# Optimization experiments

Measured on AMD Instinct MI355X. Metric: run time of the kernel, lower is better.

The kernel has to match this reference:

```python
import jax, jax.numpy as jnp
import numpy as np

B, N, DIM = 1, 512, 1024
HEADS, DH = 16, 64          # dim_head = 64, _dim = heads*dh = 1024
P = 32                      # projection_dim
P2 = P // 2
NEG_INF = -1e30


def setup_inputs() -> dict:
    key = jax.random.key(0)
    ks = jax.random.split(key, 14)
    s = 0.02
    _dim = HEADS * DH
    return {
        "x":    jax.random.normal(ks[0], (B, N, DIM), dtype=jnp.float32),
        "Wqkv": jax.random.normal(ks[1], (3 * _dim, DIM), dtype=jnp.float32) * s,
        "Wout": jax.random.normal(ks[2], (DIM, _dim), dtype=jnp.float32) * s,
        "Wq":   jax.random.normal(ks[3], (P, DH), dtype=jnp.float32) * s,
        "bq":   jax.random.normal(ks[4], (P,), dtype=jnp.float32) * s,
        "Wk":   jax.random.normal(ks[5], (P, DH), dtype=jnp.float32) * s,
        "bk":   jax.random.normal(ks[6], (P,), dtype=jnp.float32) * s,
        "W1":   jax.random.normal(ks[7], (P, 2 * P), dtype=jnp.float32) * s,
        "b1":   jax.random.normal(ks[8], (P,), dtype=jnp.float32) * s,
        "W2":   jax.random.normal(ks[9], (P2, P), dtype=jnp.float32) * s,
        "b2":   jax.random.normal(ks[10], (P2,), dtype=jnp.float32) * s,
        "W3":   jax.random.normal(ks[11], (1, P2), dtype=jnp.float32) * s,
        "b3":   jax.random.normal(ks[12], (1,), dtype=jnp.float32) * s,
    }


def reference(x, Wqkv, Wout, Wq, bq, Wk, bk, W1, b1, W2, b2, W3, b3):
    b, n, _ = x.shape
    # qkv projection, then einops 'b n (d k h) -> k b h n d' split (d outermost!)
    qkv = jnp.einsum('bnc,oc->bno', x, Wqkv).reshape(b, n, DH, 3, HEADS)
    q = jnp.transpose(qkv[:, :, :, 0, :], (0, 3, 1, 2))  # [b,h,n,dh]
    k = jnp.transpose(qkv[:, :, :, 1, :], (0, 3, 1, 2))
    v = jnp.transpose(qkv[:, :, :, 2, :], (0, 3, 1, 2))

    qp = jnp.einsum('bhnd,pd->bhnp', q, Wq) + bq  # [b,h,n,P]
    kp = jnp.einsum('bhnd,pd->bhnp', k, Wk) + bk

    # linear1 on concat(q_i, k_j): split W1 -> broadcast-add (same math,
    # avoids materializing the [b,h,n,n,2P] concat tensor)
    W1q, W1k = W1[:, :P], W1[:, P:]
    a = jnp.einsum('bhnp,qp->bhnq', qp, W1q)      # [b,h,n,P]
    c = jnp.einsum('bhnp,qp->bhnq', kp, W1k)      # [b,h,n,P]
    h1 = jax.nn.relu(a[:, :, :, None, :] + c[:, :, None, :, :] + b1)  # [b,h,n,n,P]
    h2 = jax.nn.relu(jnp.einsum('bhijp,qp->bhijq', h1, W2) + b2)      # [b,h,n,n,P/2]
    score = jnp.einsum('bhijq,oq->bhijo', h2, W3)[..., 0] + b3[0]     # [b,h,n,n]

    # causal mask (triu(1) filled with -inf)
    i = jnp.arange(n)
    causal = i[None, :] > i[:, None]
    score = jnp.where(causal, NEG_INF, score)

    attn = jax.nn.softmax(score, axis=-1)
    out = jnp.einsum('bhij,bhjd->bhid', attn, v)                      # [b,h,n,dh]
    out = jnp.transpose(out, (0, 2, 1, 3)).reshape(b, n, HEADS * DH)  # b n (h d)
    return jnp.einsum('bne,oe->bno', out, Wout)
```

## Files before the change

### kernel.cpp

```cpp
#include <hip/hip_runtime.h>
#include <hip/hip_bf16.h>
#include <hip/hip_fp16.h>
#include <math.h>

#define N_SEQ 512
#define DIM   1024
#define HEADS 16
#define DH    64
#define P     32
#define P2    16
#define PSTR  520

typedef short    bf16x8 __attribute__((ext_vector_type(8)));
typedef _Float16 f16x8  __attribute__((ext_vector_type(8)));
typedef float    f32x4  __attribute__((ext_vector_type(4)));

__device__ inline unsigned short f2bf(float f) {
  union { float f; unsigned u; } v; v.f = f;
  unsigned r = (v.u + 0x7fffu + ((v.u >> 16) & 1u)) >> 16;
  return (unsigned short)r;
}

union H8 { f16x8 v; __half2 h2[4]; unsigned u32[4]; };

__global__ __launch_bounds__(256) void prep(
    const float* __restrict__ Wqkv, const float* __restrict__ Wq,
    const float* __restrict__ bq, const float* __restrict__ Wk,
    const float* __restrict__ bk, const float* __restrict__ W1,
    const float* __restrict__ b1,
    const float* __restrict__ x, const float* __restrict__ Wout,
    short* __restrict__ Wcomb, short* __restrict__ xb,
    short* __restrict__ Woutb, float* __restrict__ ba32,
    float* __restrict__ bc32) {
  const int b = blockIdx.x, tid = threadIdx.x;
  if (b < 256) {
    __shared__ float W1s[32][33];
    __shared__ float Wqs[32][65];
    __shared__ float wsm[32][65];
    __shared__ __align__(16) float qsT[128][65];
    const int part = b >> 7, rem = b & 127;
    const int h = rem >> 3, c0 = (rem & 7) * 128;
    const int grow = part * 16 + h;
    for (int idx = tid; idx < 1024; idx += 256)
      W1s[idx >> 5][idx & 31] = W1[(idx >> 5) * 64 + part * 32 + (idx & 31)];
    const float* Wsel = part ? Wk : Wq;
    for (int idx = tid; idx < 2048; idx += 256)
      Wqs[idx >> 6][idx & 63] = Wsel[idx];
    for (int idx = tid; idx < 2048; idx += 256) {
      const int d = idx >> 5, c4 = idx & 31;
      const float4 v =
          *(const float4*)(Wqkv + (size_t)(d * 48 + grow) * DIM + c0 + c4 * 4);
      qsT[c4 * 4 + 0][d] = v.x;
      qsT[c4 * 4 + 1][d] = v.y;
      qsT[c4 * 4 + 2][d] = v.z;
      qsT[c4 * 4 + 3][d] = v.w;
    }
    __syncthreads();
    for (int idx = tid; idx < 2048; idx += 256) {
      const int q = idx >> 6, d = idx & 63;
      float s = 0.f;
#pragma unroll
      for (int p = 0; p < 32; ++p) s += W1s[q][p] * Wqs[p][d];
      wsm[q][d] = s;
    }
    __syncthreads();
    {
      const int c = tid & 127;
      float qr[64];
#pragma unroll
      for (int d4 = 0; d4 < 16; ++d4)
        *(float4*)&qr[d4 * 4] = *(const float4*)&qsT[c][d4 * 4];
#pragma unroll
      for (int step = 0; step < 16; ++step) {
        const int idx = step * 256 + tid;
        const int q = idx >> 7;
        float s = 0.f;
#pragma unroll
        for (int d = 0; d < 64; ++d) s += wsm[q][d] * qr[d];
        Wcomb[(size_t)(part * 512 + h * 32 + q) * DIM + c0 + c] = (short)f2bf(s);
      }
    }
    if (rem == 0 && tid < 32) {
      const float* bsel = part ? bk : bq;
      float s = 0.f;
#pragma unroll
      for (int p = 0; p < 32; ++p) s += W1s[tid][p] * bsel[p];
      if (part) s += b1[tid];
      (part ? bc32 : ba32)[tid] = s;
    }
  } else if (b < 384) {
#pragma unroll
    for (int rr = 0; rr < 8; ++rr) {
      const int ov = (b - 256) * 8 + rr;
      const int h = ov >> 6, d = ov & 63;
      const float4 v = *(const float4*)(Wqkv + (size_t)(d * 48 + 32 + h) * DIM + tid * 4);
      ushort4 o;
      o.x = f2bf(v.x); o.y = f2bf(v.y); o.z = f2bf(v.z); o.w = f2bf(v.w);
      *(ushort4*)(Wcomb + (size_t)(1024 + ov) * DIM + tid * 4) = o;
    }
  } else if (b < 512) {
    const int idx = (b - 384) * 256 + tid;
#pragma unroll
    for (int u = 0; u < 4; ++u) {
      const int t = u * 32768 + idx;
      const float4 v = ((const float4*)x)[t];
      ushort4 o;
      o.x = f2bf(v.x); o.y = f2bf(v.y); o.z = f2bf(v.z); o.w = f2bf(v.w);
      ((ushort4*)xb)[t] = o;
    }
  } else {
    const int idx = (b - 512) * 256 + tid;
#pragma unroll
    for (int u = 0; u < 4; ++u) {
      const int t = u * 65536 + idx;
      const float4 v = ((const float4*)Wout)[t];
      ushort4 o;
      o.x = f2bf(v.x); o.y = f2bf(v.y); o.z = f2bf(v.z); o.w = f2bf(v.w);
      ((ushort4*)Woutb)[t] = o;
    }
  }
}

__global__ __launch_bounds__(512) void gemm_acv(
    const short* __restrict__ xb, const short* __restrict__ Wcomb,
    const float* __restrict__ ba32, const float* __restrict__ bc32,
    __half* __restrict__ a_buf, __half* __restrict__ cb_buf,
    __half* __restrict__ vT) {
  const int bb = blockIdx.x;
  const int tm = bb >> 5;
  const int tn = bb & 31;
  const int w = threadIdx.x >> 6;
  const int wm = w >> 1, wn = w & 1;
  const int lane = threadIdx.x & 63;
  const int m = lane & 15, quad = lane >> 4;

  const int row0 = tm * 64 + wm * 16;
  const int col0 = tn * 64 + wn * 32;

  const short* pa  = xb + (size_t)(row0 + m) * DIM + quad * 8;
  const short* pb0 = Wcomb + (size_t)(col0 + m) * DIM + quad * 8;
  const short* pb1 = pb0 + (size_t)16 * DIM;

  bf16x8 abuf[4], b0buf[4], b1buf[4];
#pragma unroll
  for (int j = 0; j < 4; ++j) {
    abuf[j]  = *(const bf16x8*)(pa  + j * 32);
    b0buf[j] = *(const bf16x8*)(pb0 + j * 32);
    b1buf[j] = *(const bf16x8*)(pb1 + j * 32);
  }

  f32x4 acc0 = {0.f, 0.f, 0.f, 0.f}, acc1 = {0.f, 0.f, 0.f, 0.f};

#pragma unroll
  for (int ko = 0; ko < 8; ++ko) {
#pragma unroll
    for (int j = 0; j < 4; ++j) {
      const int k = ko * 4 + j;
      const bf16x8 av  = abuf[j];
      const bf16x8 b0v = b0buf[j];
      const bf16x8 b1v = b1buf[j];
      if (k + 4 < 32) {
        abuf[j]  = *(const bf16x8*)(pa  + (k + 4) * 32);
        b0buf[j] = *(const bf16x8*)(pb0 + (k + 4) * 32);
        b1buf[j] = *(const bf16x8*)(pb1 + (k + 4) * 32);
      }
      acc0 = __builtin_amdgcn_mfma_f32_16x16x32_bf16(av, b0v, acc0, 0, 0, 0);
      acc1 = __builtin_amdgcn_mfma_f32_16x16x32_bf16(av, b1v, acc1, 0, 0, 0);
    }
  }

#pragma unroll
  for (int r = 0; r < 4; ++r) {
    const int n = row0 + quad * 4 + r;
#pragma unroll
    for (int half = 0; half < 2; ++half) {
      const int o = col0 + half * 16 + m;
      const float val = half ? acc1[r] : acc0[r];
      if (o < 512) {
        const int hh = o >> 5, q = o & 31;
        a_buf[((size_t)hh * N_SEQ + n) * P + q] = __float2half(val + ba32[q]);
      } else if (o < 1024) {
        const int oo = o - 512, hh = oo >> 5, q = oo & 31;
        cb_buf[((size_t)hh * N_SEQ + n) * P + q] = __float2half(val + bc32[q]);
      } else {
        const int ov = o - 1024, hh = ov >> 6, d = ov & 63;
        vT[((size_t)hh * DH + d) * N_SEQ + n] = __float2half(val);
      }
    }
  }
}

__device__ inline float rowscore(const H8& a, const H8& c, f16x8 w2f,
                                 f32x4 b2q, float4 w3q) {
  const f16x8 z = (f16x8)(_Float16)0;
  const f16x8 u = __builtin_elementwise_max(a.v + c.v, z);
  f32x4 acc = b2q;
  acc = __builtin_amdgcn_mfma_f32_16x16x32_f16(w2f, u, acc, 0, 0, 0);
  return fmaxf(acc[0], 0.f) * w3q.x + fmaxf(acc[1], 0.f) * w3q.y
       + fmaxf(acc[2], 0.f) * w3q.z + fmaxf(acc[3], 0.f) * w3q.w;
}

__device__ inline float quadreduce4(float p0, float p1, float p2, float p3,
                                    int quad) {
  const float sx = (quad & 1) ? p0 : p1;
  const float sy = (quad & 1) ? p2 : p3;
  const float rx = __shfl_xor(sx, 16);
  const float ry = __shfl_xor(sy, 16);
  const float aa = ((quad & 1) ? p1 : p0) + rx;
  const float bb = ((quad & 1) ? p3 : p2) + ry;
  const float sz = (quad & 2) ? aa : bb;
  const float rz = __shfl_xor(sz, 32);
  return ((quad & 2) ? bb : aa) + rz;
}

__global__ __launch_bounds__(256) void attn_fused(
    const __half* __restrict__ a_g, const __half* __restrict__ cb_g,
    const float* __restrict__ W2, const float* __restrict__ b2,
    const float* __restrict__ W3,
    const __half* __restrict__ vT, short* __restrict__ attnb) {
  const int xx = blockIdx.x, yy = blockIdx.y;
  const int t = (yy & 8) ? (31 - xx) : xx;
  const int h = yy;
  const int tid = threadIdx.x;
  const int w = tid >> 6;
  const int lane = tid & 63;
  const int m = lane & 15, quad = lane >> 4;

  __shared__ __align__(16) __half probS[16][PSTR];
  __shared__ float invS[16];

  const int nj = t + 1;

  {
    f16x8 w2f;
    {
      const float4* wp = (const float4*)(W2 + m * P + quad * 8);
      const float4 w0 = wp[0], w1 = wp[1];
      H8 uu;
      uu.h2[0] = __floats2half2_rn(w0.x, w0.y);
      uu.h2[1] = __floats2half2_rn(w0.z, w0.w);
      uu.h2[2] = __floats2half2_rn(w1.x, w1.y);
      uu.h2[3] = __floats2half2_rn(w1.z, w1.w);
      w2f = uu.v;
    }
    const float4 b2f = *(const float4*)(b2 + quad * 4);
    const f32x4 b2q = {b2f.x, b2f.y, b2f.z, b2f.w};
    const float4 w3q = *(const float4*)(W3 + quad * 4);

    H8 ar[4];
#pragma unroll
    for (int r = 0; r < 4; ++r)
      ar[r].v = *(const f16x8*)(a_g + ((size_t)h * N_SEQ + t * 16 + 4 * w + r) * P + quad * 8);

    const __half* cbbase = cb_g + ((size_t)h * N_SEQ + m) * P + quad * 8;
    H8 cbn;
    cbn.v = *(const f16x8*)cbbase;
    for (int jt = 0; jt < nj; ++jt) {
      const H8 cb = cbn;
      if (jt + 1 < nj)
        cbn.v = *(const f16x8*)(cbbase + (size_t)(jt + 1) * 16 * P);
      const float s0 = rowscore(ar[0], cb, w2f, b2q, w3q);
      const float s1 = rowscore(ar[1], cb, w2f, b2q, w3q);
      const float s2 = rowscore(ar[2], cb, w2f, b2q, w3q);
      const float s3 = rowscore(ar[3], cb, w2f, b2q, w3q);
      const float fl = quadreduce4(s0, s1, s2, s3, quad);
      probS[4 * w + quad][jt * 16 + m] = __float2half(fl);
    }
  }
  __syncthreads();

  {
    const int lr = tid >> 4;
    const int c  = tid & 15;
    const int gi = t * 16 + lr;
    float mx = -1e30f;
#pragma unroll
    for (int k = 0; k < 4; ++k) {
      const int c0 = k * 128 + c * 8;
      if (c0 > gi) break;
      H8 vv; vv.v = *(const f16x8*)&probS[lr][c0];
#pragma unroll
      for (int uu = 0; uu < 8; ++uu) {
        const float s = __half2float(vv.h2[uu >> 1].data[uu & 1]);
        if (c0 + uu <= gi) mx = fmaxf(mx, s);
      }
    }
#pragma unroll
    for (int msk = 1; msk < 16; msk <<= 1) mx = fmaxf(mx, __shfl_xor(mx, msk));
    float sum = 0.f;
#pragma unroll
    for (int k = 0; k < 4; ++k) {
      const int c0 = k * 128 + c * 8;
      H8 vv; vv.v = *(const f16x8*)&probS[lr][c0];
      H8 o;
#pragma unroll
      for (int uu = 0; uu < 4; ++uu) {
        float e0 = 0.f, e1 = 0.f;
        if (c0 + 2 * uu <= gi) {
          e0 = __expf(__half2float(vv.h2[uu].data[0]) - mx);
          if (c0 + 2 * uu + 1 <= gi)
            e1 = __expf(__half2float(vv.h2[uu].data[1]) - mx);
        }
        sum += e0 + e1;
        o.h2[uu] = __floats2half2_rn(e0, e1);
      }
      *(f16x8*)&probS[lr][c0] = o.v;
    }
#pragma unroll
    for (int msk = 1; msk < 16; msk <<= 1) sum += __shfl_xor(sum, msk);
    if (c == 0) invS[lr] = 1.f / sum;
  }
  __syncthreads();

  {
    const int d0 = w * 16;
    const __half* pb = vT + ((size_t)h * DH + d0 + m) * N_SEQ + quad * 8;
    const int nk = (t + 2) >> 1;
    f32x4 acc = {0.f, 0.f, 0.f, 0.f};
    f16x8 vb = *(const f16x8*)pb;
    for (int k = 0; k < nk; ++k) {
      const f16x8 bb = vb;
      if (k + 1 < nk) vb = *(const f16x8*)(pb + (k + 1) * 32);
      const f16x8 aa = *(const f16x8*)&probS[m][k * 32 + quad * 8];
      acc = __builtin_amdgcn_mfma_f32_16x16x32_f16(aa, bb, acc, 0, 0, 0);
    }
#pragma unroll
    for (int r = 0; r < 4; ++r) {
      const int lrow = quad * 4 + r;
      const float val = acc[r] * invS[lrow];
      attnb[(size_t)(t * 16 + lrow) * DIM + h * DH + d0 + m] = (short)f2bf(val);
    }
  }
}

__global__ __launch_bounds__(512) void gemm_out16(
    const short* __restrict__ A, const short* __restrict__ B,
    float* __restrict__ C) {
  const int bb = blockIdx.x;
  const int tm = bb >> 4;
  const int tn = bb & 15;
  const int w = threadIdx.x >> 6;
  const int wm = w & 1, wn = w >> 1;
  const int lane = threadIdx.x & 63;
  const int m = lane & 15, quad = lane >> 4;

  const int row0 = tm * 32 + wm * 16;
  const int col0 = tn * 64 + wn * 16;

  const short* pa = A + (size_t)(row0 + m) * DIM + quad * 8;
  const short* pb = B + (size_t)(col0 + m) * DIM + quad * 8;

  bf16x8 abuf[4], bbuf[4];
#pragma unroll
  for (int j = 0; j < 4; ++j) {
    abuf[j] = *(const bf16x8*)(pa + j * 32);
    bbuf[j] = *(const bf16x8*)(pb + j * 32);
  }

  f32x4 acc = {0.f, 0.f, 0.f, 0.f};
#pragma unroll
  for (int ko = 0; ko < 8; ++ko) {
#pragma unroll
    for (int j = 0; j < 4; ++j) {
      const int k = ko * 4 + j;
      const bf16x8 av = abuf[j];
      const bf16x8 bv = bbuf[j];
      if (k + 4 < 32) {
        abuf[j] = *(const bf16x8*)(pa + (k + 4) * 32);
        bbuf[j] = *(const bf16x8*)(pb + (k + 4) * 32);
      }
      acc = __builtin_amdgcn_mfma_f32_16x16x32_bf16(av, bv, acc, 0, 0, 0);
    }
  }

#pragma unroll
  for (int r = 0; r < 4; ++r)
    C[(size_t)(row0 + quad * 4 + r) * DIM + col0 + m] = acc[r];
}

extern "C" void kernel_launch(void* const* d_in, const int* in_sizes, int n_in,
                              void* d_out, int out_size, void* d_ws, size_t ws_size,
                              hipStream_t stream) {
  const float* x    = (const float*)d_in[0];
  const float* Wqkv = (const float*)d_in[1];
  const float* Wout = (const float*)d_in[2];
  const float* Wq   = (const float*)d_in[3];
  const float* bq   = (const float*)d_in[4];
  const float* Wk   = (const float*)d_in[5];
  const float* bk   = (const float*)d_in[6];
  const float* W1   = (const float*)d_in[7];
  const float* b1   = (const float*)d_in[8];
  const float* W2   = (const float*)d_in[9];
  const float* b2   = (const float*)d_in[10];
  const float* W3   = (const float*)d_in[11];
  float* out = (float*)d_out;

  float*  ws     = (float*)d_ws;
  float*  ba32   = ws;
  float*  bc32   = ba32 + 32;
  __half* a_buf  = (__half*)(bc32 + 32);
  __half* cb_buf = a_buf + (size_t)HEADS * N_SEQ * P;
  __half* vT     = cb_buf + (size_t)HEADS * N_SEQ * P;
  short*  Wcomb  = (short*)(vT + (size_t)HEADS * DH * N_SEQ);
  short*  xb     = Wcomb + (size_t)2048 * DIM;
  short*  Woutb  = xb + (size_t)N_SEQ * DIM;
  short*  attnb  = Woutb + (size_t)DIM * DIM;

  prep<<<768, 256, 0, stream>>>(Wqkv, Wq, bq, Wk, bk, W1, b1, x, Wout,
                                Wcomb, xb, Woutb, ba32, bc32);

  gemm_acv<<<256, 512, 0, stream>>>(xb, Wcomb, ba32, bc32, a_buf, cb_buf, vT);

  dim3 g3(32, HEADS);
  attn_fused<<<g3, 256, 0, stream>>>(a_buf, cb_buf, W2, b2, W3, vT, attnb);

  gemm_out16<<<256, 512, 0, stream>>>(attnb, Woutb, out);
}
```

Baseline: 160.0 us.

## Fuse fp32-to-half conversion of x, V weights and Wout into GEMM loads

Removes the separate bf16 conversion passes over x, the V part of Wqkv and Wout from the prep kernel. The GEMM kernels now load fp32 directly and convert to fp16 in registers with packed cvt before issuing f16 MFMA. The precision for all GEMMs and the attention output also moves from bf16 to fp16. This cuts prep-kernel work and the intermediate global round-trips. In exchange the GEMM inner loops load twice the bytes per element and do extra conversion ALU work.

```diff
diff --git a/kernel.cpp b/kernel.cpp
--- a/kernel.cpp
+++ b/kernel.cpp
@@ -11,118 +11,88 @@
 #define P2    16
 #define PSTR  520
 
-typedef short    bf16x8 __attribute__((ext_vector_type(8)));
-typedef _Float16 f16x8  __attribute__((ext_vector_type(8)));
-typedef float    f32x4  __attribute__((ext_vector_type(4)));
-
-__device__ inline unsigned short f2bf(float f) {
-  union { float f; unsigned u; } v; v.f = f;
-  unsigned r = (v.u + 0x7fffu + ((v.u >> 16) & 1u)) >> 16;
-  return (unsigned short)r;
-}
+typedef _Float16 f16x8 __attribute__((ext_vector_type(8)));
+typedef __fp16   h16x2 __attribute__((ext_vector_type(2)));
+typedef float    f32x4 __attribute__((ext_vector_type(4)));
 
 union H8 { f16x8 v; __half2 h2[4]; unsigned u32[4]; };
+
+__device__ inline f16x8 cvt8(const float4 a, const float4 b) {
+  union { f16x8 v; h16x2 p[4]; } u;
+  u.p[0] = __builtin_amdgcn_cvt_pkrtz(a.x, a.y);
+  u.p[1] = __builtin_amdgcn_cvt_pkrtz(a.z, a.w);
+  u.p[2] = __builtin_amdgcn_cvt_pkrtz(b.x, b.y);
+  u.p[3] = __builtin_amdgcn_cvt_pkrtz(b.z, b.w);
+  return u.v;
+}
 
 __global__ __launch_bounds__(256) void prep(
     const float* __restrict__ Wqkv, const float* __restrict__ Wq,
     const float* __restrict__ bq, const float* __restrict__ Wk,
     const float* __restrict__ bk, const float* __restrict__ W1,
     const float* __restrict__ b1,
-    const float* __restrict__ x, const float* __restrict__ Wout,
-    short* __restrict__ Wcomb, short* __restrict__ xb,
-    short* __restrict__ Woutb, float* __restrict__ ba32,
+    __half* __restrict__ Wcomb, float* __restrict__ ba32,
     float* __restrict__ bc32) {
   const int b = blockIdx.x, tid = threadIdx.x;
-  if (b < 256) {
-    __shared__ float W1s[32][33];
-    __shared__ float Wqs[32][65];
-    __shared__ float wsm[32][65];
-    __shared__ __align__(16) float qsT[128][65];
-    const int part = b >> 7, rem = b & 127;
-    const int h = rem >> 3, c0 = (rem & 7) * 128;
-    const int grow = part * 16 + h;
-    for (int idx = tid; idx < 1024; idx += 256)
-      W1s[idx >> 5][idx & 31] = W1[(idx >> 5) * 64 + part * 32 + (idx & 31)];
-    const float* Wsel = part ? Wk : Wq;
-    for (int idx = tid; idx < 2048; idx += 256)
-      Wqs[idx >> 6][idx & 63] = Wsel[idx];
-    for (int idx = tid; idx < 2048; idx += 256) {
-      const int d = idx >> 5, c4 = idx & 31;
-      const float4 v =
-          *(const float4*)(Wqkv + (size_t)(d * 48 + grow) * DIM + c0 + c4 * 4);
-      qsT[c4 * 4 + 0][d] = v.x;
-      qsT[c4 * 4 + 1][d] = v.y;
-      qsT[c4 * 4 + 2][d] = v.z;
-      qsT[c4 * 4 + 3][d] = v.w;
-    }
-    __syncthreads();
-    for (int idx = tid; idx < 2048; idx += 256) {
-      const int q = idx >> 6, d = idx & 63;
+  __shared__ float W1s[32][33];
+  __shared__ float Wqs[32][65];
+  __shared__ float wsm[32][65];
+  __shared__ __align__(16) float qsT[128][65];
+  const int part = b >> 7, rem = b & 127;
+  const int h = rem >> 3, c0 = (rem & 7) * 128;
+  const int grow = part * 16 + h;
+  for (int idx = tid; idx < 1024; idx += 256)
+    W1s[idx >> 5][idx & 31] = W1[(idx >> 5) * 64 + part * 32 + (idx & 31)];
+  const float* Wsel = part ? Wk : Wq;
+  for (int idx = tid; idx < 2048; idx += 256)
+    Wqs[idx >> 6][idx & 63] = Wsel[idx];
+  for (int idx = tid; idx < 2048; idx += 256) {
+    const int d = idx >> 5, c4 = idx & 31;
+    const float4 v =
+        *(const float4*)(Wqkv + (size_t)(d * 48 + grow) * DIM + c0 + c4 * 4);
+    qsT[c4 * 4 + 0][d] = v.x;
+    qsT[c4 * 4 + 1][d] = v.y;
+    qsT[c4 * 4 + 2][d] = v.z;
+    qsT[c4 * 4 + 3][d] = v.w;
+  }
+  __syncthreads();
+  for (int idx = tid; idx < 2048; idx += 256) {
+    const int q = idx >> 6, d = idx & 63;
+    float s = 0.f;
+#pragma unroll
+    for (int pp = 0; pp < 32; ++pp) s += W1s[q][pp] * Wqs[pp][d];
+    wsm[q][d] = s;
+  }
+  __syncthreads();
+  {
+    const int c = tid & 127;
+    float qr[64];
+#pragma unroll
+    for (int d4 = 0; d4 < 16; ++d4)
+      *(float4*)&qr[d4 * 4] = *(const float4*)&qsT[c][d4 * 4];
+#pragma unroll
+    for (int step = 0; step < 16; ++step) {
+      const int idx = step * 256 + tid;
+      const int q = idx >> 7;
       float s = 0.f;
 #pragma unroll
-      for (int p = 0; p < 32; ++p) s += W1s[q][p] * Wqs[p][d];
-      wsm[q][d] = s;
-    }
-    __syncthreads();
-    {
-      const int c = tid & 127;
-      float qr[64];
-#pragma unroll
-      for (int d4 = 0; d4 < 16; ++d4)
-        *(float4*)&qr[d4 * 4] = *(const float4*)&qsT[c][d4 * 4];
-#pragma unroll
-      for (int step = 0; step < 16; ++step) {
-        const int idx = step * 256 + tid;
-        const int q = idx >> 7;
-        float s = 0.f;
-#pragma unroll
-        for (int d = 0; d < 64; ++d) s += wsm[q][d] * qr[d];
-        Wcomb[(size_t)(part * 512 + h * 32 + q) * DIM + c0 + c] = (short)f2bf(s);
-      }
-    }
-    if (rem == 0 && tid < 32) {
-      const float* bsel = part ? bk : bq;
-      float s = 0.f;
-#pragma unroll
-      for (int p = 0; p < 32; ++p) s += W1s[tid][p] * bsel[p];
-      if (part) s += b1[tid];
-      (part ? bc32 : ba32)[tid] = s;
-    }
-  } else if (b < 384) {
-#pragma unroll
-    for (int rr = 0; rr < 8; ++rr) {
-      const int ov = (b - 256) * 8 + rr;
-      const int h = ov >> 6, d = ov & 63;
-      const float4 v = *(const float4*)(Wqkv + (size_t)(d * 48 + 32 + h) * DIM + tid * 4);
-      ushort4 o;
-      o.x = f2bf(v.x); o.y = f2bf(v.y); o.z = f2bf(v.z); o.w = f2bf(v.w);
-      *(ushort4*)(Wcomb + (size_t)(1024 + ov) * DIM + tid * 4) = o;
-    }
-  } else if (b < 512) {
-    const int idx = (b - 384) * 256 + tid;
-#pragma unroll
-    for (int u = 0; u < 4; ++u) {
-      const int t = u * 32768 + idx;
-      const float4 v = ((const float4*)x)[t];
-      ushort4 o;
-      o.x = f2bf(v.x); o.y = f2bf(v.y); o.z = f2bf(v.z); o.w = f2bf(v.w);
-      ((ushort4*)xb)[t] = o;
-    }
-  } else {
-    const int idx = (b - 512) * 256 + tid;
-#pragma unroll
-    for (int u = 0; u < 4; ++u) {
-      const int t = u * 65536 + idx;
-      const float4 v = ((const float4*)Wout)[t];
-      ushort4 o;
-      o.x = f2bf(v.x); o.y = f2bf(v.y); o.z = f2bf(v.z); o.w = f2bf(v.w);
-      ((ushort4*)Woutb)[t] = o;
-    }
+      for (int d = 0; d < 64; ++d) s += wsm[q][d] * qr[d];
+      Wcomb[(size_t)(part * 512 + h * 32 + q) * DIM + c0 + c] = __float2half(s);
+    }
+  }
+  if (rem == 0 && tid < 32) {
+    const float* bsel = part ? bk : bq;
+    float s = 0.f;
+#pragma unroll
+    for (int pp = 0; pp < 32; ++pp) s += W1s[tid][pp] * bsel[pp];
+    if (part) s += b1[tid];
+    (part ? bc32 : ba32)[tid] = s;
   }
 }
 
 __global__ __launch_bounds__(512) void gemm_acv(
-    const short* __restrict__ xb, const short* __restrict__ Wcomb,
+    const float* __restrict__ x, const __half* __restrict__ Wcomb,
+    const float* __restrict__ Wqkv,
     const float* __restrict__ ba32, const float* __restrict__ bc32,
     __half* __restrict__ a_buf, __half* __restrict__ cb_buf,
     __half* __restrict__ vT) {
@@ -137,35 +107,78 @@
   const int row0 = tm * 64 + wm * 16;
   const int col0 = tn * 64 + wn * 32;
 
-  const short* pa  = xb + (size_t)(row0 + m) * DIM + quad * 8;
-  const short* pb0 = Wcomb + (size_t)(col0 + m) * DIM + quad * 8;
-  const short* pb1 = pb0 + (size_t)16 * DIM;
-
-  bf16x8 abuf[4], b0buf[4], b1buf[4];
+  const float* pa = x + (size_t)(row0 + m) * DIM + quad * 8;
+
+  float4 araw[4][2];
 #pragma unroll
   for (int j = 0; j < 4; ++j) {
-    abuf[j]  = *(const bf16x8*)(pa  + j * 32);
-    b0buf[j] = *(const bf16x8*)(pb0 + j * 32);
-    b1buf[j] = *(const bf16x8*)(pb1 + j * 32);
+    araw[j][0] = *(const float4*)(pa + j * 32);
+    araw[j][1] = *(const float4*)(pa + j * 32 + 4);
   }
 
   f32x4 acc0 = {0.f, 0.f, 0.f, 0.f}, acc1 = {0.f, 0.f, 0.f, 0.f};
 
-#pragma unroll
-  for (int ko = 0; ko < 8; ++ko) {
+  if (tn < 16) {
+    const __half* pb0 = Wcomb + (size_t)(col0 + m) * DIM + quad * 8;
+    const __half* pb1 = pb0 + (size_t)16 * DIM;
+    f16x8 b0buf[4], b1buf[4];
 #pragma unroll
     for (int j = 0; j < 4; ++j) {
-      const int k = ko * 4 + j;
-      const bf16x8 av  = abuf[j];
-      const bf16x8 b0v = b0buf[j];
-      const bf16x8 b1v = b1buf[j];
-      if (k + 4 < 32) {
-        abuf[j]  = *(const bf16x8*)(pa  + (k + 4) * 32);
-        b0buf[j] = *(const bf16x8*)(pb0 + (k + 4) * 32);
-        b1buf[j] = *(const bf16x8*)(pb1 + (k + 4) * 32);
-      }
-      acc0 = __builtin_amdgcn_mfma_f32_16x16x32_bf16(av, b0v, acc0, 0, 0, 0);
-      acc1 = __builtin_amdgcn_mfma_f32_16x16x32_bf16(av, b1v, acc1, 0, 0, 0);
+      b0buf[j] = *(const f16x8*)(pb0 + j * 32);
+      b1buf[j] = *(const f16x8*)(pb1 + j * 32);
+    }
+#pragma unroll
+    for (int ko = 0; ko < 8; ++ko) {
+#pragma unroll
+      for (int j = 0; j < 4; ++j) {
+        const int k = ko * 4 + j;
+        const f16x8 av  = cvt8(araw[j][0], araw[j][1]);
+        const f16x8 b0v = b0buf[j];
+        const f16x8 b1v = b1buf[j];
+        if (k + 4 < 32) {
+          araw[j][0] = *(const float4*)(pa + (k + 4) * 32);
+          araw[j][1] = *(const float4*)(pa + (k + 4) * 32 + 4);
+          b0buf[j]   = *(const f16x8*)(pb0 + (k + 4) * 32);
+          b1buf[j]   = *(const f16x8*)(pb1 + (k + 4) * 32);
+        }
+        acc0 = __builtin_amdgcn_mfma_f32_16x16x32_f16(av, b0v, acc0, 0, 0, 0);
+        acc1 = __builtin_amdgcn_mfma_f32_16x16x32_f16(av, b1v, acc1, 0, 0, 0);
+      }
+    }
+  } else {
+    const int rv0 = col0 + m - 1024;
+    const int rv1 = rv0 + 16;
+    const float* pb0 =
+        Wqkv + (size_t)((rv0 & 63) * 48 + 32 + (rv0 >> 6)) * DIM + quad * 8;
+    const float* pb1 =
+        Wqkv + (size_t)((rv1 & 63) * 48 + 32 + (rv1 >> 6)) * DIM + quad * 8;
+    float4 b0raw[4][2], b1raw[4][2];
+#pragma unroll
+    for (int j = 0; j < 4; ++j) {
+      b0raw[j][0] = *(const float4*)(pb0 + j * 32);
+      b0raw[j][1] = *(const float4*)(pb0 + j * 32 + 4);
+      b1raw[j][0] = *(const float4*)(pb1 + j * 32);
+      b1raw[j][1] = *(const float4*)(pb1 + j * 32 + 4);
+    }
+#pragma unroll
+    for (int ko = 0; ko < 8; ++ko) {
+#pragma unroll
+      for (int j = 0; j < 4; ++j) {
+        const int k = ko * 4 + j;
+        const f16x8 av  = cvt8(araw[j][0], araw[j][1]);
+        const f16x8 b0v = cvt8(b0raw[j][0], b0raw[j][1]);
+        const f16x8 b1v = cvt8(b1raw[j][0], b1raw[j][1]);
+        if (k + 4 < 32) {
+          araw[j][0]  = *(const float4*)(pa + (k + 4) * 32);
+          araw[j][1]  = *(const float4*)(pa + (k + 4) * 32 + 4);
+          b0raw[j][0] = *(const float4*)(pb0 + (k + 4) * 32);
+          b0raw[j][1] = *(const float4*)(pb0 + (k + 4) * 32 + 4);
+          b1raw[j][0] = *(const float4*)(pb1 + (k + 4) * 32);
+          b1raw[j][1] = *(const float4*)(pb1 + (k + 4) * 32 + 4);
+        }
+        acc0 = __builtin_amdgcn_mfma_f32_16x16x32_f16(av, b0v, acc0, 0, 0, 0);
+        acc1 = __builtin_amdgcn_mfma_f32_16x16x32_f16(av, b1v, acc1, 0, 0, 0);
+      }
     }
   }
 
@@ -217,7 +230,7 @@
     const __half* __restrict__ a_g, const __half* __restrict__ cb_g,
     const float* __restrict__ W2, const float* __restrict__ b2,
     const float* __restrict__ W3,
-    const __half* __restrict__ vT, short* __restrict__ attnb) {
+    const __half* __restrict__ vT, __half* __restrict__ attnb) {
   const int xx = blockIdx.x, yy = blockIdx.y;
   const int t = (yy & 8) ? (31 - xx) : xx;
   const int h = yy;
@@ -328,13 +341,13 @@
     for (int r = 0; r < 4; ++r) {
       const int lrow = quad * 4 + r;
       const float val = acc[r] * invS[lrow];
-      attnb[(size_t)(t * 16 + lrow) * DIM + h * DH + d0 + m] = (short)f2bf(val);
+      attnb[(size_t)(t * 16 + lrow) * DIM + h * DH + d0 + m] = __float2half(val);
     }
   }
 }
 
 __global__ __launch_bounds__(512) void gemm_out16(
-    const short* __restrict__ A, const short* __restrict__ B,
+    const __half* __restrict__ A, const float* __restrict__ Wout,
     float* __restrict__ C) {
   const int bb = blockIdx.x;
   const int tm = bb >> 4;
@@ -347,14 +360,16 @@
   const int row0 = tm * 32 + wm * 16;
   const int col0 = tn * 64 + wn * 16;
 
-  const short* pa = A + (size_t)(row0 + m) * DIM + quad * 8;
-  const short* pb = B + (size_t)(col0 + m) * DIM + quad * 8;
-
-  bf16x8 abuf[4], bbuf[4];
+  const __half* pa = A + (size_t)(row0 + m) * DIM + quad * 8;
+  const float*  pb = Wout + (size_t)(col0 + m) * DIM + quad * 8;
+
+  f16x8 abuf[4];
+  float4 braw[4][2];
 #pragma unroll
   for (int j = 0; j < 4; ++j) {
-    abuf[j] = *(const bf16x8*)(pa + j * 32);
-    bbuf[j] = *(const bf16x8*)(pb + j * 32);
+    abuf[j]    = *(const f16x8*)(pa + j * 32);
+    braw[j][0] = *(const float4*)(pb + j * 32);
+    braw[j][1] = *(const float4*)(pb + j * 32 + 4);
   }
 
   f32x4 acc = {0.f, 0.f, 0.f, 0.f};
@@ -363,13 +378,14 @@
 #pragma unroll
     for (int j = 0; j < 4; ++j) {
       const int k = ko * 4 + j;
-      const bf16x8 av = abuf[j];
-      const bf16x8 bv = bbuf[j];
+      const f16x8 av = abuf[j];
+      const f16x8 bv = cvt8(braw[j][0], braw[j][1]);
       if (k + 4 < 32) {
-        abuf[j] = *(const bf16x8*)(pa + (k + 4) * 32);
-        bbuf[j] = *(const bf16x8*)(pb + (k + 4) * 32);
-      }
-      acc = __builtin_amdgcn_mfma_f32_16x16x32_bf16(av, bv, acc, 0, 0, 0);
+        abuf[j]    = *(const f16x8*)(pa + (k + 4) * 32);
+        braw[j][0] = *(const float4*)(pb + (k + 4) * 32);
+        braw[j][1] = *(const float4*)(pb + (k + 4) * 32 + 4);
+      }
+      acc = __builtin_amdgcn_mfma_f32_16x16x32_f16(av, bv, acc, 0, 0, 0);
     }
   }
 
@@ -401,18 +417,17 @@
   __half* a_buf  = (__half*)(bc32 + 32);
   __half* cb_buf = a_buf + (size_t)HEADS * N_SEQ * P;
   __half* vT     = cb_buf + (size_t)HEADS * N_SEQ * P;
-  short*  Wcomb  = (short*)(vT + (size_t)HEADS * DH * N_SEQ);
-  short*  xb     = Wcomb + (size_t)2048 * DIM;
-  short*  Woutb  = xb + (size_t)N_SEQ * DIM;
-  short*  attnb  = Woutb + (size_t)DIM * DIM;
-
-  prep<<<768, 256, 0, stream>>>(Wqkv, Wq, bq, Wk, bk, W1, b1, x, Wout,
-                                Wcomb, xb, Woutb, ba32, bc32);
-
-  gemm_acv<<<256, 512, 0, stream>>>(xb, Wcomb, ba32, bc32, a_buf, cb_buf, vT);
+  __half* Wcomb  = vT + (size_t)HEADS * DH * N_SEQ;
+  __half* attnb  = Wcomb + (size_t)1024 * DIM;
+
+  prep<<<256, 256, 0, stream>>>(Wqkv, Wq, bq, Wk, bk, W1, b1,
+                                Wcomb, ba32, bc32);
+
+  gemm_acv<<<256, 512, 0, stream>>>(x, Wcomb, Wqkv, ba32, bc32,
+                                    a_buf, cb_buf, vT);
 
   dim3 g3(32, HEADS);
   attn_fused<<<g3, 256, 0, stream>>>(a_buf, cb_buf, W2, b2, W3, vT, attnb);
 
-  gemm_out16<<<256, 512, 0, stream>>>(attnb, Woutb, out);
-}
+  gemm_out16<<<256, 512, 0, stream>>>(attnb, Wout, out);
+}
```

After: 186.9 us. +16.8%, slower.
